# Optimization experiments

Hardware: AMD Instinct MI355X
Metric: run time of the kernel (lower is better)

## Reference

```python
import jax, jax.numpy as jnp
import numpy as np

N = 20000      # nodes
E = 320000     # edges
H = 128        # hidden_channels
F = 128        # num_filters
R = 50         # num_rbf
L = 6          # num_interactions
CU = 5.0       # cutoff_upper (cutoff_lower = 0)
ZMAX = 100


def cosine_cutoff(d):
    return 0.5 * (jnp.cos(d * jnp.pi / CU) + 1.0) * (d < CU).astype(d.dtype)


def expnorm_rbf(d, means, betas):
    # d: [E] -> [E, R]
    de = d[:, None]
    return cosine_cutoff(de) * jnp.exp(-betas * (jnp.exp(-de) - means) ** 2)


def setup_inputs() -> dict:
    key = jax.random.key(0)
    ks = jax.random.split(key, 24)
    s = 0.05
    inp = {
        "z": jax.random.randint(ks[0], (N,), 0, ZMAX),
        "edge_index": jax.random.randint(ks[1], (2, E), 0, N),
        "edge_weight": jax.random.uniform(ks[2], (E,), jnp.float32) * CU,
        # embedding + rbf params
        "emb": jax.random.normal(ks[3], (ZMAX, H), jnp.float32) * s,
        "means": jnp.linspace(np.exp(-CU), 1.0, R).astype(jnp.float32),
        "betas": jnp.full((R,), (2.0 / R * (1.0 - np.exp(-CU))) ** -2, jnp.float32),
        # neighbor embedding params (Linear stored as [in, out])
        "dp_w": jax.random.normal(ks[4], (R, H), jnp.float32) * s,
        "dp_b": jnp.zeros((H,), jnp.float32),
        "comb_w": jax.random.normal(ks[5], (2 * H, H), jnp.float32) * s,
        "comb_b": jnp.zeros((H,), jnp.float32),
        # per-layer interaction params, stacked over L
        "mlp_w1": jax.random.normal(ks[6], (L, R, F), jnp.float32) * s,
        "mlp_b1": jnp.zeros((L, F), jnp.float32),
        "mlp_w2": jax.random.normal(ks[7], (L, F, F), jnp.float32) * s,
        "mlp_b2": jnp.zeros((L, F), jnp.float32),
        "lin1_w": jax.random.normal(ks[8], (L, H, F), jnp.float32) * s,  # no bias
        "lin2_w": jax.random.normal(ks[9], (L, F, H), jnp.float32) * s,
        "lin2_b": jnp.zeros((L, H), jnp.float32),
        "lin_w": jax.random.normal(ks[10], (L, H, H), jnp.float32) * s,
        "lin_b": jnp.zeros((L, H), jnp.float32),
    }
    return inp


def reference(z, edge_index, edge_weight, emb, means, betas, dp_w, dp_b,
              comb_w, comb_b, mlp_w1, mlp_b1, mlp_w2, mlp_b2,
              lin1_w, lin2_w, lin2_b, lin_w, lin_b):
    j = edge_index[0]  # source (x_j gathered here)
    i = edge_index[1]  # target (aggregation index)

    C = cosine_cutoff(edge_weight)                 # [E]
    attr = expnorm_rbf(edge_weight, means, betas)  # [E, R]

    x = emb[z]                                     # [N, H]

    # --- NeighborEmbedding (aggr='add') ---
    Wn = (attr @ dp_w + dp_b) * C[:, None]         # [E, H]
    agg = jax.ops.segment_sum(x[j] * Wn, i, num_segments=N)
    x = jnp.concatenate([x, agg], axis=1) @ comb_w + comb_b

    # mean-aggregation denominator (PyG mean: 0 for isolated nodes)
    cnt = jax.ops.segment_sum(jnp.ones((E,), x.dtype), i, num_segments=N)
    inv_cnt = jnp.where(cnt > 0, 1.0 / jnp.maximum(cnt, 1.0), 0.0)[:, None]

    # --- Interaction blocks with residual ---
    for l in range(L):
        W = jax.nn.silu(attr @ mlp_w1[l] + mlp_b1[l]) @ mlp_w2[l] + mlp_b2[l]
        W = W * C[:, None]                         # [E, F]
        h = x @ lin1_w[l]                          # [N, F]
        h = jax.ops.segment_sum(h[j] * W, i, num_segments=N) * inv_cnt
        h = h @ lin2_w[l] + lin2_b[l]
        h = jax.nn.silu(h)
        h = h @ lin_w[l] + lin_b[l]
        x = x + h
    return x
```

## Files before the change

### kernel.cpp

```cpp
#include <hip/hip_runtime.h>
#include <hip/hip_bf16.h>
#include <math.h>

#define N_NODES 20000
#define N_EDGES 320000
#define NTILES  5000
#define HD 128
#define RD 50
#define NL 6
#define CUTV 5.0f
#define PI_F 3.14159265358979323846f
#define WPAD 132

typedef __attribute__((ext_vector_type(8))) short short8;
typedef __attribute__((ext_vector_type(4))) float f32x4;

__device__ __forceinline__ float cutoff_f(float d) {
  float c = 0.5f * (__cosf(d * (PI_F / CUTV)) + 1.0f);
  return d < CUTV ? c : 0.0f;
}
__device__ __forceinline__ float silu_f(float x) {
  return x / (1.0f + __expf(-x));
}
__device__ __forceinline__ unsigned short bf16bits(float f) {
  union { __hip_bfloat16 b; unsigned short u; } cv;
  cv.b = __float2bfloat16(f);
  return cv.u;
}
__device__ __forceinline__ float bfu_hi(unsigned int bits_in_high) {
  union { unsigned int u; float f; } v; v.u = bits_in_high; return v.f;
}
__device__ __forceinline__ f32x4 mfma16(short8 a, short8 b, f32x4 c) {
  return __builtin_amdgcn_mfma_f32_16x16x32_bf16(a, b, c, 0, 0, 0);
}
__device__ __forceinline__ void split8(const float* __restrict__ p,
                                       short8& h, short8& l) {
  float4 v0 = *(const float4*)p;
  float4 v1 = *(const float4*)(p + 4);
  float vv[8] = {v0.x, v0.y, v0.z, v0.w, v1.x, v1.y, v1.z, v1.w};
  #pragma unroll
  for (int i = 0; i < 8; ++i) {
    unsigned short hb = bf16bits(vv[i]);
    h[i] = (short)hb;
    l[i] = (short)bf16bits(vv[i] - bfu_hi((unsigned int)hb << 16));
  }
}

__global__ void k_hist(const int* __restrict__ ei, int* __restrict__ deg) {
  int e = blockIdx.x * blockDim.x + threadIdx.x;
  if (e < N_EDGES) atomicAdd(&deg[ei[N_EDGES + e]], 1);
}

__global__ void k_scan(const int* __restrict__ deg, int* __restrict__ rowptr,
                       int* __restrict__ cursor) {
  __shared__ int s[1024];
  __shared__ int run;
  int t = threadIdx.x;
  if (t == 0) run = 0;
  __syncthreads();
  for (int base = 0; base < N_NODES; base += 1024) {
    int idx = base + t;
    int v = (idx < N_NODES) ? deg[idx] : 0;
    s[t] = v;
    __syncthreads();
    for (int off = 1; off < 1024; off <<= 1) {
      int add = (t >= off) ? s[t - off] : 0;
      __syncthreads();
      s[t] += add;
      __syncthreads();
    }
    int excl = s[t] - v;
    int r = run;
    if (idx < N_NODES) { rowptr[idx] = r + excl; cursor[idx] = r + excl; }
    __syncthreads();
    if (t == 0) run += s[1023];
    __syncthreads();
  }
  if (t == 0) rowptr[N_NODES] = run;
}

__global__ void k_scatter(const int* __restrict__ ei, int* __restrict__ cursor,
                          int* __restrict__ eids) {
  int e = blockIdx.x * blockDim.x + threadIdx.x;
  if (e < N_EDGES) {
    int i = ei[N_EDGES + e];
    int p = atomicAdd(&cursor[i], 1);
    eids[p] = e;
  }
}

__global__ void k_init(const int* __restrict__ z, const float* __restrict__ emb,
                       float* __restrict__ x) {
  int idx = blockIdx.x * blockDim.x + threadIdx.x;
  if (idx < N_NODES * 32) {
    int n = idx >> 5, c4 = idx & 31;
    float4 v = ((const float4*)emb)[z[n] * 32 + c4];
    ((float4*)x)[n * 32 + c4] = v;
  }
}

__global__ __launch_bounds__(256)
void k_attr(const int* __restrict__ ei, const float* __restrict__ ew,
            const int* __restrict__ eids, const int* __restrict__ rowptr,
            const float* __restrict__ means, const float* __restrict__ betas,
            unsigned short* __restrict__ attr_fr, float* __restrict__ Csrt,
            float* __restrict__ Cinv, int* __restrict__ srcj) {
  int gid = blockIdx.x * blockDim.x + threadIdx.x;
  int tile = gid >> 9, s = gid & 511;
  int kg = s >> 6, e = s & 63;
  int p = tile * 64 + e;
  int eo = eids[p];
  float d = ew[eo];
  float C = cutoff_f(d);
  float ex = __expf(-d);
  short8 out;
  #pragma unroll
  for (int i = 0; i < 8; ++i) {
    int k = kg * 8 + i;
    float v = 0.0f;
    if (k < RD) {
      float em = ex - means[k];
      v = C * __expf(-betas[k] * em * em);
    }
    out[i] = (short)bf16bits(v);
  }
  *(short8*)(attr_fr + (size_t)gid * 8) = out;
  if (kg == 0) {
    Csrt[p] = C;
    srcj[p] = ei[eo];
    int dn = ei[N_EDGES + eo];
    int dg = rowptr[dn + 1] - rowptr[dn];
    Cinv[p] = C / (float)(dg > 0 ? dg : 1);
  }
}

template <bool TWO>
__global__ __launch_bounds__(256, 4)
void k_filter(const unsigned short* __restrict__ afr_g,
              const float* __restrict__ scale_e,
              const float* __restrict__ w1g, const float* __restrict__ b1g,
              const float* __restrict__ w2g, const float* __restrict__ bFg,
              unsigned short* __restrict__ Wout) {
  __shared__ unsigned short s_u[64 * WPAD];
  int t = threadIdx.x;
  int wv = t >> 6, lane = t & 63;
  int c = lane & 15, g = lane >> 4;

  short8 B1[2][2];
  #pragma unroll
  for (int ntl = 0; ntl < 2; ++ntl) {
    int col = (2 * wv + ntl) * 16 + c;
    #pragma unroll
    for (int kt = 0; kt < 2; ++kt) {
      short8 v;
      #pragma unroll
      for (int i = 0; i < 8; ++i) {
        int k = 32 * kt + 8 * g + i;
        v[i] = (k < RD) ? (short)bf16bits(w1g[k * HD + col]) : (short)0;
      }
      B1[ntl][kt] = v;
    }
  }
  short8 B2[2][4];
  if (TWO) {
    #pragma unroll
    for (int ntl = 0; ntl < 2; ++ntl) {
      int col = (2 * wv + ntl) * 16 + c;
      #pragma unroll
      for (int kt = 0; kt < 4; ++kt) {
        short8 v;
        #pragma unroll
        for (int i = 0; i < 8; ++i) {
          int k = 32 * kt + 8 * g + i;
          v[i] = (short)bf16bits(w2g[k * HD + col]);
        }
        B2[ntl][kt] = v;
      }
    }
  }
  float b1v[2], bFv[2];
  #pragma unroll
  for (int ntl = 0; ntl < 2; ++ntl) {
    int col = (2 * wv + ntl) * 16 + c;
    b1v[ntl] = TWO ? b1g[col] : 0.0f;
    bFv[ntl] = bFg[col];
  }

  for (int tile = blockIdx.x; tile < NTILES; tile += gridDim.x) {
    const unsigned short* afr = afr_g + (size_t)tile * 4096;
    f32x4 acc[4][2];
    #pragma unroll
    for (int mt = 0; mt < 4; ++mt) {
      acc[mt][0] = (f32x4){0.f, 0.f, 0.f, 0.f};
      acc[mt][1] = (f32x4){0.f, 0.f, 0.f, 0.f};
    }
    #pragma unroll
    for (int kt = 0; kt < 2; ++kt) {
      #pragma unroll
      for (int mt = 0; mt < 4; ++mt) {
        short8 a = *(const short8*)(afr + ((size_t)((4 * kt + g) * 64 + (16 * mt + c))) * 8);
        acc[mt][0] = mfma16(a, B1[0][kt], acc[mt][0]);
        acc[mt][1] = mfma16(a, B1[1][kt], acc[mt][1]);
      }
    }
    if (TWO) {
      #pragma unroll
      for (int mt = 0; mt < 4; ++mt) {
        #pragma unroll
        for (int ntl = 0; ntl < 2; ++ntl) {
          int ch = (2 * wv + ntl) * 16 + c;
          #pragma unroll
          for (int r = 0; r < 4; ++r) {
            int e = 16 * mt + 4 * g + r;
            float v = silu_f(acc[mt][ntl][r] + b1v[ntl]);
            s_u[((ch >> 3) * 64 + e) * 8 + (ch & 7)] = bf16bits(v);
          }
        }
      }
      __syncthreads();
      #pragma unroll
      for (int mt = 0; mt < 4; ++mt) {
        acc[mt][0] = (f32x4){0.f, 0.f, 0.f, 0.f};
        acc[mt][1] = (f32x4){0.f, 0.f, 0.f, 0.f};
      }
      #pragma unroll
      for (int kt = 0; kt < 4; ++kt) {
        #pragma unroll
        for (int mt = 0; mt < 4; ++mt) {
          short8 a = *(const short8*)(s_u + ((4 * kt + g) * 64 + (16 * mt + c)) * 8);
          acc[mt][0] = mfma16(a, B2[0][kt], acc[mt][0]);
          acc[mt][1] = mfma16(a, B2[1][kt], acc[mt][1]);
        }
      }
      __syncthreads();
    }
    #pragma unroll
    for (int mt = 0; mt < 4; ++mt) {
      float Cv[4];
      #pragma unroll
      for (int r = 0; r < 4; ++r) Cv[r] = scale_e[tile * 64 + 16 * mt + 4 * g + r];
      #pragma unroll
      for (int ntl = 0; ntl < 2; ++ntl) {
        int ch = (2 * wv + ntl) * 16 + c;
        #pragma unroll
        for (int r = 0; r < 4; ++r) {
          int e = 16 * mt + 4 * g + r;
          float v = (acc[mt][ntl][r] + bFv[ntl]) * Cv[r];
          s_u[e * WPAD + ch] = bf16bits(v);
        }
      }
    }
    __syncthreads();
    {
      short8* dst = (short8*)(Wout + (size_t)tile * 8192);
      #pragma unroll
      for (int k2 = 0; k2 < 4; ++k2) {
        int m = t + 256 * k2;
        int e = m >> 4, chunk = m & 15;
        dst[m] = *(const short8*)(s_u + e * WPAD + chunk * 8);
      }
    }
    __syncthreads();
  }
}

__global__ __launch_bounds__(256)
void k_segsum(const unsigned short* __restrict__ Wst, const float* __restrict__ h,
              const int* __restrict__ rowptr, const int* __restrict__ srcj,
              float* __restrict__ out) {
  int t = threadIdx.x, wv = t >> 6, lane = t & 63;
  int n = blockIdx.x * 4 + wv;
  if (n >= N_NODES) return;
  int half = lane >> 5;
  int q = lane & 31;
  int beg = rowptr[n], end = rowptr[n + 1];
  float a0 = 0.f, a1 = 0.f, a2 = 0.f, a3 = 0.f;
  #pragma unroll 4
  for (int p = beg + half; p < end; p += 2) {
    int j = srcj[p];
    uint2 wb = *(const uint2*)(Wst + (size_t)p * 128 + 4 * q);
    float4 hv = *(const float4*)(h + (size_t)j * 128 + 4 * q);
    a0 += hv.x * bfu_hi(wb.x << 16);
    a1 += hv.y * bfu_hi(wb.x & 0xffff0000u);
    a2 += hv.z * bfu_hi(wb.y << 16);
    a3 += hv.w * bfu_hi(wb.y & 0xffff0000u);
  }
  a0 += __shfl_xor(a0, 32, 64);
  a1 += __shfl_xor(a1, 32, 64);
  a2 += __shfl_xor(a2, 32, 64);
  a3 += __shfl_xor(a3, 32, 64);
  if (half == 0) {
    *(float4*)(out + (size_t)n * 128 + 4 * q) = make_float4(a0, a1, a2, a3);
  }
}

template <int KT, bool HASB, bool SILU, bool ADD>
__global__ __launch_bounds__(512)
void k_nmfma(const float* __restrict__ in1, const float* __restrict__ in2,
             const float* __restrict__ Wg, const float* __restrict__ bias,
             float* __restrict__ out) {
  int t = threadIdx.x;
  int wv = t >> 6, lane = t & 63;
  int c = lane & 15, g = lane >> 4;
  int col = 16 * wv + c;
  int n0 = blockIdx.x * 32;

  short8 Bh[KT], Bl[KT];
  #pragma unroll
  for (int kt = 0; kt < KT; ++kt) {
    short8 h, l;
    #pragma unroll
    for (int i = 0; i < 8; ++i) {
      int k = 32 * kt + 8 * g + i;
      float w = Wg[(size_t)k * HD + col];
      unsigned short hb = bf16bits(w);
      h[i] = (short)hb;
      l[i] = (short)bf16bits(w - bfu_hi((unsigned int)hb << 16));
    }
    Bh[kt] = h; Bl[kt] = l;
  }

  f32x4 acc[2];
  acc[0] = (f32x4){0.f, 0.f, 0.f, 0.f};
  acc[1] = (f32x4){0.f, 0.f, 0.f, 0.f};

  #pragma unroll
  for (int kt = 0; kt < KT; ++kt) {
    const float* in = (KT == 8 && kt >= 4) ? in2 : in1;
    int koff = (kt & 3) * 32 + 8 * g;
    #pragma unroll
    for (int mt = 0; mt < 2; ++mt) {
      int row = n0 + 16 * mt + c;
      int rowc = row < N_NODES ? row : N_NODES - 1;
      short8 ah, al;
      split8(in + (size_t)rowc * HD + koff, ah, al);
      acc[mt] = mfma16(ah, Bh[kt], acc[mt]);
      acc[mt] = mfma16(al, Bh[kt], acc[mt]);
      acc[mt] = mfma16(ah, Bl[kt], acc[mt]);
    }
  }
  __syncthreads();
  float bv = HASB ? bias[col] : 0.0f;
  #pragma unroll
  for (int mt = 0; mt < 2; ++mt) {
    #pragma unroll
    for (int r = 0; r < 4; ++r) {
      int row = n0 + 16 * mt + 4 * g + r;
      if (row < N_NODES) {
        float v = acc[mt][r] + bv;
        if (SILU) v = silu_f(v);
        if (ADD) out[(size_t)row * HD + col] += v;
        else out[(size_t)row * HD + col] = v;
      }
    }
  }
}

__global__ __launch_bounds__(512)
void k_nmfma2(const float* __restrict__ in1,
              const float* __restrict__ W1, const float* __restrict__ b1,
              const float* __restrict__ W2, const float* __restrict__ b2,
              float* __restrict__ xout) {
  __shared__ unsigned short s_uh[4096];
  __shared__ unsigned short s_ul[4096];
  int t = threadIdx.x;
  int wv = t >> 6, lane = t & 63;
  int c = lane & 15, g = lane >> 4;
  int col = 16 * wv + c;
  int n0 = blockIdx.x * 32;

  short8 B1h[4], B1l[4], B2h[4], B2l[4];
  #pragma unroll
  for (int kt = 0; kt < 4; ++kt) {
    short8 h1, l1, h2, l2;
    #pragma unroll
    for (int i = 0; i < 8; ++i) {
      int k = 32 * kt + 8 * g + i;
      float w = W1[(size_t)k * HD + col];
      unsigned short hb = bf16bits(w);
      h1[i] = (short)hb;
      l1[i] = (short)bf16bits(w - bfu_hi((unsigned int)hb << 16));
      float w2 = W2[(size_t)k * HD + col];
      unsigned short hb2 = bf16bits(w2);
      h2[i] = (short)hb2;
      l2[i] = (short)bf16bits(w2 - bfu_hi((unsigned int)hb2 << 16));
    }
    B1h[kt] = h1; B1l[kt] = l1; B2h[kt] = h2; B2l[kt] = l2;
  }
  float b1v = b1[col], b2v = b2[col];

  f32x4 acc[2];
  acc[0] = (f32x4){0.f, 0.f, 0.f, 0.f};
  acc[1] = (f32x4){0.f, 0.f, 0.f, 0.f};
  #pragma unroll
  for (int kt = 0; kt < 4; ++kt) {
    int koff = kt * 32 + 8 * g;
    #pragma unroll
    for (int mt = 0; mt < 2; ++mt) {
      int row = n0 + 16 * mt + c;
      int rowc = row < N_NODES ? row : N_NODES - 1;
      short8 ah, al;
      split8(in1 + (size_t)rowc * HD + koff, ah, al);
      acc[mt] = mfma16(ah, B1h[kt], acc[mt]);
      acc[mt] = mfma16(al, B1h[kt], acc[mt]);
      acc[mt] = mfma16(ah, B1l[kt], acc[mt]);
    }
  }
  #pragma unroll
  for (int mt = 0; mt < 2; ++mt) {
    #pragma unroll
    for (int r = 0; r < 4; ++r) {
      int e = 16 * mt + 4 * g + r;
      float v = silu_f(acc[mt][r] + b1v);
      unsigned short hb = bf16bits(v);
      unsigned short lb = bf16bits(v - bfu_hi((unsigned int)hb << 16));
      int idx = ((col >> 3) * 32 + e) * 8 + (col & 7);
      s_uh[idx] = hb;
      s_ul[idx] = lb;
    }
  }
  __syncthreads();
  acc[0] = (f32x4){0.f, 0.f, 0.f, 0.f};
  acc[1] = (f32x4){0.f, 0.f, 0.f, 0.f};
  #pragma unroll
  for (int kt = 0; kt < 4; ++kt) {
    #pragma unroll
    for (int mt = 0; mt < 2; ++mt) {
      int idx = ((4 * kt + g) * 32 + (16 * mt + c)) * 8;
      short8 ah = *(const short8*)(s_uh + idx);
      short8 al = *(const short8*)(s_ul + idx);
      acc[mt] = mfma16(ah, B2h[kt], acc[mt]);
      acc[mt] = mfma16(al, B2h[kt], acc[mt]);
      acc[mt] = mfma16(ah, B2l[kt], acc[mt]);
    }
  }
  #pragma unroll
  for (int mt = 0; mt < 2; ++mt) {
    #pragma unroll
    for (int r = 0; r < 4; ++r) {
      int row = n0 + 16 * mt + 4 * g + r;
      if (row < N_NODES) {
        xout[(size_t)row * HD + col] += acc[mt][r] + b2v;
      }
    }
  }
}

extern "C" void kernel_launch(void* const* d_in, const int* in_sizes, int n_in,
                              void* d_out, int out_size, void* d_ws, size_t ws_size,
                              hipStream_t stream) {
  const int* z = (const int*)d_in[0];
  const int* ei = (const int*)d_in[1];
  const float* ew = (const float*)d_in[2];
  const float* emb = (const float*)d_in[3];
  const float* means = (const float*)d_in[4];
  const float* betas = (const float*)d_in[5];
  const float* dp_w = (const float*)d_in[6];
  const float* dp_b = (const float*)d_in[7];
  const float* comb_w = (const float*)d_in[8];
  const float* comb_b = (const float*)d_in[9];
  const float* mlp_w1 = (const float*)d_in[10];
  const float* mlp_b1 = (const float*)d_in[11];
  const float* mlp_w2 = (const float*)d_in[12];
  const float* mlp_b2 = (const float*)d_in[13];
  const float* lin1_w = (const float*)d_in[14];
  const float* lin2_w = (const float*)d_in[15];
  const float* lin2_b = (const float*)d_in[16];
  const float* lin_w = (const float*)d_in[17];
  const float* lin_b = (const float*)d_in[18];
  float* x = (float*)d_out;

  int* rowptr = (int*)d_ws;
  int* deg = rowptr + 20032;
  int* cursor = deg + 20032;
  int* eids = cursor + 20032;
  int* srcj = eids + N_EDGES;
  float* Csrt = (float*)(srcj + N_EDGES);
  float* Cinv = Csrt + N_EDGES;
  unsigned short* attr_fr = (unsigned short*)(Cinv + N_EDGES);
  unsigned short* Wst = attr_fr + (size_t)N_EDGES * 64;
  float* hbuf = (float*)(Wst + (size_t)N_EDGES * 128);
  float* aggb = hbuf + (size_t)N_NODES * HD;

  hipMemsetAsync(deg, 0, N_NODES * sizeof(int), stream);
  k_hist<<<(N_EDGES + 255) / 256, 256, 0, stream>>>(ei, deg);
  k_scan<<<1, 1024, 0, stream>>>(deg, rowptr, cursor);
  k_scatter<<<(N_EDGES + 255) / 256, 256, 0, stream>>>(ei, cursor, eids);
  k_attr<<<NTILES * 2, 256, 0, stream>>>(ei, ew, eids, rowptr, means, betas,
                                         attr_fr, Csrt, Cinv, srcj);
  k_init<<<(N_NODES * 32 + 255) / 256, 256, 0, stream>>>(z, emb, x);

  k_filter<false><<<2500, 256, 0, stream>>>(attr_fr, Csrt, dp_w, nullptr,
                                            nullptr, dp_b, Wst);
  k_segsum<<<5000, 256, 0, stream>>>(Wst, x, rowptr, srcj, aggb);
  k_nmfma<8, true, false, false><<<625, 512, 0, stream>>>(x, aggb, comb_w,
                                                          comb_b, x);

  for (int l = 0; l < NL; ++l) {
    k_nmfma<4, false, false, false><<<625, 512, 0, stream>>>(
        x, nullptr, lin1_w + (size_t)l * HD * HD, nullptr, hbuf);
    k_filter<true><<<2500, 256, 0, stream>>>(
        attr_fr, Cinv,
        mlp_w1 + (size_t)l * RD * HD, mlp_b1 + (size_t)l * HD,
        mlp_w2 + (size_t)l * HD * HD, mlp_b2 + (size_t)l * HD, Wst);
    k_segsum<<<5000, 256, 0, stream>>>(Wst, hbuf, rowptr, srcj, aggb);
    k_nmfma2<<<625, 512, 0, stream>>>(
        aggb, lin2_w + (size_t)l * HD * HD, lin2_b + (size_t)l * HD,
        lin_w + (size_t)l * HD * HD, lin_b + (size_t)l * HD, x);
  }
}
```

Measured before the change: 896.0 us.

## Parallelize degree scan across blocks and double filter kernel grid/occupancy

```diff
diff --git a/kernel.cpp b/kernel.cpp
--- a/kernel.cpp
+++ b/kernel.cpp
@@ -11,6 +11,7 @@
 #define CUTV 5.0f
 #define PI_F 3.14159265358979323846f
 #define WPAD 132
+#define SCAN_B 79
 
 typedef __attribute__((ext_vector_type(8))) short short8;
 typedef __attribute__((ext_vector_type(4))) float f32x4;
@@ -51,32 +52,47 @@
   if (e < N_EDGES) atomicAdd(&deg[ei[N_EDGES + e]], 1);
 }
 
-__global__ void k_scan(const int* __restrict__ deg, int* __restrict__ rowptr,
-                       int* __restrict__ cursor) {
-  __shared__ int s[1024];
-  __shared__ int run;
-  int t = threadIdx.x;
-  if (t == 0) run = 0;
+__global__ void k_bsum(const int* __restrict__ deg, int* __restrict__ bsum) {
+  __shared__ int sdata[256];
+  int b = blockIdx.x, t = threadIdx.x;
+  int i = b * 256 + t;
+  sdata[t] = (i < N_NODES) ? deg[i] : 0;
   __syncthreads();
-  for (int base = 0; base < N_NODES; base += 1024) {
-    int idx = base + t;
-    int v = (idx < N_NODES) ? deg[idx] : 0;
-    s[t] = v;
+  for (int off = 128; off > 0; off >>= 1) {
+    if (t < off) sdata[t] += sdata[t + off];
     __syncthreads();
-    for (int off = 1; off < 1024; off <<= 1) {
-      int add = (t >= off) ? s[t - off] : 0;
-      __syncthreads();
-      s[t] += add;
-      __syncthreads();
-    }
-    int excl = s[t] - v;
-    int r = run;
-    if (idx < N_NODES) { rowptr[idx] = r + excl; cursor[idx] = r + excl; }
+  }
+  if (t == 0) bsum[b] = sdata[0];
+}
+
+__global__ void k_bscan(const int* __restrict__ bsum, int* __restrict__ boff,
+                        int* __restrict__ rowptrN) {
+  if (threadIdx.x == 0) {
+    int run = 0;
+    for (int b = 0; b < SCAN_B; ++b) { boff[b] = run; run += bsum[b]; }
+    rowptrN[0] = run;
+  }
+}
+
+__global__ void k_scanout(const int* __restrict__ deg, const int* __restrict__ boff,
+                          int* __restrict__ rowptr, int* __restrict__ cursor) {
+  __shared__ int sdata[256];
+  int b = blockIdx.x, t = threadIdx.x;
+  int i = b * 256 + t;
+  int v = (i < N_NODES) ? deg[i] : 0;
+  sdata[t] = v;
+  __syncthreads();
+  for (int off = 1; off < 256; off <<= 1) {
+    int add = (t >= off) ? sdata[t - off] : 0;
     __syncthreads();
-    if (t == 0) run += s[1023];
+    sdata[t] += add;
     __syncthreads();
   }
-  if (t == 0) rowptr[N_NODES] = run;
+  if (i < N_NODES) {
+    int excl = boff[b] + sdata[t] - v;
+    rowptr[i] = excl;
+    cursor[i] = excl;
+  }
 }
 
 __global__ void k_scatter(const int* __restrict__ ei, int* __restrict__ cursor,
@@ -135,7 +151,7 @@
 }
 
 template <bool TWO>
-__global__ __launch_bounds__(256, 4)
+__global__ __launch_bounds__(256, 8)
 void k_filter(const unsigned short* __restrict__ afr_g,
               const float* __restrict__ scale_e,
               const float* __restrict__ w1g, const float* __restrict__ b1g,
@@ -473,7 +489,9 @@
   int* rowptr = (int*)d_ws;
   int* deg = rowptr + 20032;
   int* cursor = deg + 20032;
-  int* eids = cursor + 20032;
+  int* bsum = cursor + 20032;
+  int* boff = bsum + 128;
+  int* eids = boff + 128;
   int* srcj = eids + N_EDGES;
   float* Csrt = (float*)(srcj + N_EDGES);
   float* Cinv = Csrt + N_EDGES;
@@ -484,13 +502,15 @@
 
   hipMemsetAsync(deg, 0, N_NODES * sizeof(int), stream);
   k_hist<<<(N_EDGES + 255) / 256, 256, 0, stream>>>(ei, deg);
-  k_scan<<<1, 1024, 0, stream>>>(deg, rowptr, cursor);
+  k_bsum<<<SCAN_B, 256, 0, stream>>>(deg, bsum);
+  k_bscan<<<1, 64, 0, stream>>>(bsum, boff, rowptr + N_NODES);
+  k_scanout<<<SCAN_B, 256, 0, stream>>>(deg, boff, rowptr, cursor);
   k_scatter<<<(N_EDGES + 255) / 256, 256, 0, stream>>>(ei, cursor, eids);
   k_attr<<<NTILES * 2, 256, 0, stream>>>(ei, ew, eids, rowptr, means, betas,
                                          attr_fr, Csrt, Cinv, srcj);
   k_init<<<(N_NODES * 32 + 255) / 256, 256, 0, stream>>>(z, emb, x);
 
-  k_filter<false><<<2500, 256, 0, stream>>>(attr_fr, Csrt, dp_w, nullptr,
+  k_filter<false><<<5000, 256, 0, stream>>>(attr_fr, Csrt, dp_w, nullptr,
                                             nullptr, dp_b, Wst);
   k_segsum<<<5000, 256, 0, stream>>>(Wst, x, rowptr, srcj, aggb);
   k_nmfma<8, true, false, false><<<625, 512, 0, stream>>>(x, aggb, comb_w,
@@ -499,7 +519,7 @@
   for (int l = 0; l < NL; ++l) {
     k_nmfma<4, false, false, false><<<625, 512, 0, stream>>>(
         x, nullptr, lin1_w + (size_t)l * HD * HD, nullptr, hbuf);
-    k_filter<true><<<2500, 256, 0, stream>>>(
+    k_filter<true><<<5000, 256, 0, stream>>>(
         attr_fr, Cinv,
         mlp_w1 + (size_t)l * RD * HD, mlp_b1 + (size_t)l * HD,
         mlp_w2 + (size_t)l * HD * HD, mlp_b2 + (size_t)l * HD, Wst);
```

After: 1.813 ms. +102.3%, slower.
